# Kernel optimization log

Measured on AMD Instinct MI355X. Metric: run time of the kernel, lower is better.

Reference implementation:

```python
import jax, jax.numpy as jnp
import numpy as np

B, T, C, H = 4, 2048, 1024, 16
D = C // H  # head_dim = 64


def setup_inputs() -> dict:
    key = jax.random.key(0)
    k1, k2, k3 = jax.random.split(key, 3)
    x = jax.random.normal(k1, (B, T, C), dtype=jnp.float32)
    # torch Linear init ~ U(-1/sqrt(fan_in), 1/sqrt(fan_in)); scaled normal is fine for a baseline
    w_qkv = jax.random.normal(k2, (C, 3 * C), dtype=jnp.float32) * (1.0 / np.sqrt(C))
    w_proj = jax.random.normal(k3, (C, C), dtype=jnp.float32) * (1.0 / np.sqrt(C))
    return {"x": x, "w_qkv": w_qkv, "w_proj": w_proj}


def reference(x, w_qkv, w_proj):
    Bb, Tt, Cc = x.shape
    qkv = x @ w_qkv                                   # [B,T,3C]
    q, k, v = jnp.split(qkv, 3, axis=-1)
    # [B,T,C] -> [B,H,T,D]
    q = q.reshape(Bb, Tt, H, D).transpose(0, 2, 1, 3)
    k = k.reshape(Bb, Tt, H, D).transpose(0, 2, 1, 3)
    v = v.reshape(Bb, Tt, H, D).transpose(0, 2, 1, 3)
    scale = 1.0 / np.sqrt(D).astype(np.float32)
    logits = jnp.einsum("bhqd,bhkd->bhqk", q, k) * scale  # [B,H,T,T]
    causal = jnp.tril(jnp.ones((Tt, Tt), dtype=bool))
    logits = jnp.where(causal, logits, jnp.finfo(logits.dtype).min)
    attn = jax.nn.softmax(logits, axis=-1)
    y = jnp.einsum("bhqk,bhkd->bhqd", attn, v)            # [B,H,T,D]
    y = y.transpose(0, 2, 1, 3).reshape(Bb, Tt, Cc)
    return y @ w_proj                                     # dropout p=0 (eval)
```

## Files before the change

### kernel.cpp

```cpp
#include <hip/hip_runtime.h>
#include <hip/hip_bf16.h>
#include <stdint.h>

typedef unsigned short u16;
typedef __attribute__((ext_vector_type(4))) float f32x4;
typedef __attribute__((ext_vector_type(16))) float f32x16;
typedef __attribute__((ext_vector_type(8))) __bf16 bf16x8;
typedef __attribute__((ext_vector_type(2))) unsigned int u32x2;

__device__ __forceinline__ u16 f2bf(float f) {
  union { float f; uint32_t u; } x; x.f = f;
  const uint32_t u = x.u;
  return (u16)((u + 0x7fffu + ((u >> 16) & 1u)) >> 16);
}

#define QSCALE 0.1803368801111244f

__global__ void cvt_f32_bf16(const float* __restrict__ in, u16* __restrict__ out,
                             int n) {
  const int i = (blockIdx.x * blockDim.x + threadIdx.x) * 4;
  if (i < n) {
    const float4 v = *(const float4*)(in + i);
    ushort4 o;
    o.x = f2bf(v.x); o.y = f2bf(v.y); o.z = f2bf(v.z); o.w = f2bf(v.w);
    *(ushort4*)(out + i) = o;
  }
}

__global__ void transpose_cvt(const float* __restrict__ in, u16* __restrict__ out,
                              int R, int Cc) {
  __shared__ u16 tile[64][66];
  const int tx = threadIdx.x, ty = threadIdx.y;
  const int c0 = blockIdx.x * 64, r0 = blockIdx.y * 64;
#pragma unroll
  for (int i = 0; i < 4; ++i)
    tile[ty + i * 16][tx] = f2bf(in[(size_t)(r0 + ty + i * 16) * Cc + c0 + tx]);
  __syncthreads();
#pragma unroll
  for (int i = 0; i < 4; ++i)
    out[(size_t)(c0 + ty + i * 16) * R + r0 + tx] = tile[tx][ty + i * 16];
}

__global__ void transpose_v(const u16* __restrict__ V, u16* __restrict__ VT) {
  __shared__ u16 tile[64][66];
  const int tx = threadIdx.x, ty = threadIdx.y;
  const int r0 = blockIdx.x * 64;
  const size_t ho = (size_t)blockIdx.y * 2048 * 64;
  const u16* in = V + ho;
  u16* out = VT + ho;
#pragma unroll
  for (int i = 0; i < 4; ++i)
    tile[ty + i * 16][tx] = in[(size_t)(r0 + ty + i * 16) * 64 + tx];
  __syncthreads();
#pragma unroll
  for (int i = 0; i < 4; ++i)
    out[(size_t)(ty + i * 16) * 2048 + r0 + tx] = tile[tx][ty + i * 16];
}

__global__ __launch_bounds__(512, 2) void gemm8p_qkv(
    const u16* __restrict__ A, const u16* __restrict__ BT,
    u16* __restrict__ Qo, u16* __restrict__ Ko, u16* __restrict__ Vo,
    int K) {
  __shared__ u16 L[2][2][2][128 * 64];
  const int tid = threadIdx.x, wid = tid >> 6, lane = tid & 63;
  const int wm = wid >> 2, wn = wid & 3;
  const int l15 = lane & 15, l4 = lane >> 4;
  const int bn = blockIdx.x, bm = blockIdx.y;

  const u16* Atile = A + (size_t)bm * 256 * K;
  const u16* Btile = BT + (size_t)bn * 256 * K;

  f32x4 acc[8][4] = {};
  bf16x8 aF[4][2], bF[4][2];
  const int cb = wid * 64 + lane;

#define SB8() __builtin_amdgcn_sched_barrier(0)
#define BAR8() { SB8(); __builtin_amdgcn_s_barrier(); SB8(); }
#define VW4() { SB8(); asm volatile("s_waitcnt vmcnt(4)" ::: "memory"); SB8(); }
#define STG(d, op, h, kt) { \
    const u16* s0_ = ((op) ? Btile : Atile) + (size_t)(h) * 128 * K + (size_t)(kt) * 64; \
    _Pragma("unroll") for (int j_ = 0; j_ < 2; ++j_) { \
      const int c_ = j_ * 512 + cb; \
      const int r_ = c_ >> 3; \
      const int g_ = (c_ & 7) ^ (r_ & 7); \
      __builtin_amdgcn_global_load_lds( \
          (const __attribute__((address_space(1))) uint32_t*)(s0_ + (size_t)r_ * K + g_ * 8), \
          (__attribute__((address_space(3))) uint32_t*)(&L[d][op][h][(j_ * 512 + wid * 64) * 8]), 16, 0, 0); \
    } }
#define LD_A(d, mbase) { \
    _Pragma("unroll") for (int m_ = 0; m_ < 4; ++m_) \
    _Pragma("unroll") for (int k_ = 0; k_ < 2; ++k_) \
      aF[m_][k_] = *(const bf16x8*)&L[d][0][wm][(((mbase) + m_) * 16 + l15) * 64 + (((k_ * 4 + l4) ^ (l15 & 7)) * 8)]; }
#define LD_B(d, nbase) { \
    _Pragma("unroll") for (int n_ = 0; n_ < 2; ++n_) \
    _Pragma("unroll") for (int k_ = 0; k_ < 2; ++k_) \
      bF[(nbase) + n_][k_] = *(const bf16x8*)&L[d][1][wn >> 1][((wn & 1) * 64 + ((nbase) + n_) * 16 + l15) * 64 + (((k_ * 4 + l4) ^ (l15 & 7)) * 8)]; }
#define MQ(MS, NS) { __builtin_amdgcn_s_setprio(1); \
    _Pragma("unroll") for (int m_ = 0; m_ < 4; ++m_) \
    _Pragma("unroll") for (int n_ = 0; n_ < 2; ++n_) \
    _Pragma("unroll") for (int kk_ = 0; kk_ < 2; ++kk_) \
      acc[(MS) * 4 + m_][(NS) * 2 + n_] = __builtin_amdgcn_mfma_f32_16x16x32_bf16( \
          aF[m_][kk_], bF[(NS) * 2 + n_][kk_], acc[(MS) * 4 + m_][(NS) * 2 + n_], 0, 0, 0); \
    __builtin_amdgcn_s_setprio(0); }

  STG(0, 1, 0, 0); STG(0, 0, 0, 0); STG(0, 1, 1, 0); STG(0, 0, 1, 0);
  STG(1, 1, 0, 1); STG(1, 0, 0, 1);
  VW4();
  BAR8();

  const int nkt = K >> 6;
  for (int it = 0; it < nkt / 2; ++it) {
    const int t1 = 2 * it + 1;
    const int t2 = (2 * it + 2 < nkt) ? 2 * it + 2 : nkt - 1;
    const int t3 = (2 * it + 3 < nkt) ? 2 * it + 3 : nkt - 1;
    LD_A(0, 0); LD_B(0, 0);
    STG(1, 1, 1, t1);
    BAR8(); MQ(0, 0); BAR8();
    LD_B(0, 2);
    STG(1, 0, 1, t1);
    BAR8(); MQ(0, 1); BAR8();
    LD_A(0, 4);
    STG(0, 1, 0, t2);
    BAR8(); MQ(1, 0); BAR8();
    STG(0, 0, 0, t2);
    VW4();
    BAR8(); MQ(1, 1); BAR8();
    LD_A(1, 0); LD_B(1, 0);
    STG(0, 1, 1, t2);
    BAR8(); MQ(0, 0); BAR8();
    LD_B(1, 2);
    STG(0, 0, 1, t2);
    BAR8(); MQ(0, 1); BAR8();
    LD_A(1, 4);
    STG(1, 1, 0, t3);
    BAR8(); MQ(1, 0); BAR8();
    STG(1, 0, 0, t3);
    VW4();
    BAR8(); MQ(1, 1); BAR8();
  }
  asm volatile("s_waitcnt vmcnt(0)" ::: "memory");

  const int row0 = bm * 256 + wm * 128;
  const int col0 = bn * 256 + wn * 64;
#pragma unroll
  for (int m = 0; m < 8; ++m) {
#pragma unroll
    for (int n = 0; n < 4; ++n) {
#pragma unroll
      for (int jj = 0; jj < 4; ++jj) {
        const int row = row0 + m * 16 + l4 * 4 + jj;
        const int col = col0 + n * 16 + l15;
        const int sec = col >> 10, c = col & 1023;
        const int h = c >> 6, d = c & 63;
        const int b = row >> 11, t = row & 2047;
        float av = acc[m][n][jj];
        if (sec == 0) av *= QSCALE;
        u16* dst = (sec == 0) ? Qo : (sec == 1) ? Ko : Vo;
        dst[(((size_t)(b * 16 + h)) * 2048 + t) * 64 + d] = f2bf(av);
      }
    }
  }
#undef SB8
#undef BAR8
#undef VW4
#undef STG
#undef LD_A
#undef LD_B
#undef MQ
}

__global__ __launch_bounds__(256) void gemm_bt(
    const u16* __restrict__ A, const u16* __restrict__ BT,
    float* __restrict__ out, int M, int N, int K) {
  __shared__ u16 Asm_[128 * 32];
  __shared__ u16 Bsm_[128 * 32];
  const int tid = threadIdx.x;
  const int wid = tid >> 6, lane = tid & 63;
  const int wm = wid >> 1, wn = wid & 1;
  const int l15 = lane & 15, l4 = lane >> 4;
  const int bm = blockIdx.y, bn = blockIdx.x;

  const u16* Ag = A + (size_t)bm * 128 * K;
  const u16* Bg = BT + (size_t)bn * 128 * K;

  f32x4 acc[4][4] = {};

  const int srow = lane >> 2;
  const int scol = (lane & 3) * 8;

  for (int kt = 0; kt < K; kt += 32) {
    __syncthreads();
#pragma unroll
    for (int it = 0; it < 2; ++it) {
      const int c = it * 4 + wid;
      const int row = c * 16 + srow;
      __builtin_amdgcn_global_load_lds(
          (const __attribute__((address_space(1))) uint32_t*)(Ag + (size_t)row * K + kt + scol),
          (__attribute__((address_space(3))) uint32_t*)(&Asm_[c * 512]), 16, 0, 0);
      __builtin_amdgcn_global_load_lds(
          (const __attribute__((address_space(1))) uint32_t*)(Bg + (size_t)row * K + kt + scol),
          (__attribute__((address_space(3))) uint32_t*)(&Bsm_[c * 512]), 16, 0, 0);
    }
    __syncthreads();

    bf16x8 af[4], bfr[4];
#pragma unroll
    for (int m = 0; m < 4; ++m)
      af[m] = *(const bf16x8*)&Asm_[(wm * 64 + m * 16 + l15) * 32 + l4 * 8];
#pragma unroll
    for (int n = 0; n < 4; ++n)
      bfr[n] = *(const bf16x8*)&Bsm_[(wn * 64 + n * 16 + l15) * 32 + l4 * 8];
#pragma unroll
    for (int m = 0; m < 4; ++m)
#pragma unroll
      for (int n = 0; n < 4; ++n)
        acc[m][n] = __builtin_amdgcn_mfma_f32_16x16x32_bf16(af[m], bfr[n], acc[m][n], 0, 0, 0);
  }

  const int row0 = bm * 128 + wm * 64;
  const int col0 = bn * 128 + wn * 64;
#pragma unroll
  for (int m = 0; m < 4; ++m)
#pragma unroll
    for (int n = 0; n < 4; ++n)
#pragma unroll
      for (int j = 0; j < 4; ++j) {
        const int row = row0 + m * 16 + l4 * 4 + j;
        const int col = col0 + n * 16 + l15;
        out[(size_t)row * N + col] = acc[m][n][j];
      }
}

__global__ __launch_bounds__(256, 4) void attn_fwd(const u16* __restrict__ Qp,
                                                   const u16* __restrict__ Kp,
                                                   const u16* __restrict__ VTp,
                                                   u16* __restrict__ Y) {
  constexpr int DP = 72;
  constexpr float THR = 11.0f;
  __shared__ u16 Ks[2][64 * DP];
  __shared__ u16 Vt[2][64 * DP];

  const int xorm = (int)((0x0A050F00u >> ((blockIdx.y >> 4) * 8)) & 15u);
  const int qt = (int)blockIdx.x ^ xorm;
  const int bh = blockIdx.y;
  const int b = bh >> 4, h = bh & 15;
  const int tid = threadIdx.x, lane = tid & 63;
  const int wid = tid >> 6;
  const int l31 = lane & 31, hb = lane >> 5;

  const size_t head_off = (size_t)bh * 2048 * 64;
  const u16* Kh = Kp + head_off;
  const u16* VTh = VTp + head_off;

  const int qg = qt * 128 + wid * 32 + l31;
  const u16* Qrow = Qp + head_off + (size_t)qg * 64;

  bf16x8 qf[4];
#pragma unroll
  for (int d = 0; d < 4; ++d)
    qf[d] = *(const bf16x8*)(Qrow + d * 16 + hb * 8);

  float m_ = -1e30f, l_ = 0.f;
  f32x16 oacc[2] = {};

  const int sr = tid >> 3;
  const int sc = (tid & 7) * 8;

  bf16x8 kreg[2], vreg[2];
  auto kvload = [&](int kt) {
#pragma unroll
    for (int it = 0; it < 2; ++it) {
      const int r = sr + it * 32;
      kreg[it] = *(const bf16x8*)(Kh + (size_t)(kt * 64 + r) * 64 + sc);
      vreg[it] = *(const bf16x8*)(VTh + (size_t)r * 2048 + kt * 64 + sc);
    }
  };
  auto kvwrite = [&](int buf) {
#pragma unroll
    for (int it = 0; it < 2; ++it) {
      const int r = sr + it * 32;
      *(bf16x8*)&Ks[buf][r * DP + sc] = kreg[it];
      *(bf16x8*)&Vt[buf][r * DP + sc] = vreg[it];
    }
  };

  kvload(0);
  kvwrite(0);
  __syncthreads();

  const int nt = 2 * qt + 2;
  for (int kt = 0; kt < nt; ++kt) {
    const int cur = kt & 1;
    const bool havenext = (kt + 1 < nt);
    if (havenext) kvload(kt + 1);

    const bool diag = (kt >= 2 * qt);

#pragma unroll
    for (int kb2 = 0; kb2 < 2; ++kb2) {
      f32x16 s = {};
      __builtin_amdgcn_s_setprio(1);
#pragma unroll
      for (int d = 0; d < 4; ++d) {
        const bf16x8 kf = *(const bf16x8*)&Ks[cur][(kb2 * 32 + l31) * DP + d * 16 + hb * 8];
        s = __builtin_amdgcn_mfma_f32_32x32x16_bf16(kf, qf[d], s, 0, 0, 0);
      }
      __builtin_amdgcn_s_setprio(0);

      if (diag) {
        const int kbase = kt * 64 + kb2 * 32 + hb * 4;
#pragma unroll
        for (int r = 0; r < 16; ++r) {
          const int koff = (r & 3) + 8 * (r >> 2);
          if (kbase + koff > qg) s[r] = -1e30f;
        }
      }

      float pmax = s[0];
#pragma unroll
      for (int r = 1; r < 16; ++r) pmax = fmaxf(pmax, s[r]);
      if (!__all(pmax - m_ <= THR)) {
        const float fm = fmaxf(pmax, __shfl_xor(pmax, 32));
        const float mnew = fmaxf(m_, fm);
        const float alpha = __builtin_exp2f(m_ - mnew);
        m_ = mnew;
        l_ *= alpha;
#pragma unroll
        for (int nb = 0; nb < 2; ++nb)
#pragma unroll
          for (int r = 0; r < 16; ++r) oacc[nb][r] *= alpha;
      }
#pragma unroll
      for (int r = 0; r < 16; ++r) {
        s[r] = __builtin_exp2f(s[r] - m_);
        l_ += s[r];
      }

      bf16x8 pb[2];
#pragma unroll
      for (int st = 0; st < 2; ++st) {
        uint32_t x0, x1, y0, y1;
        asm("v_cvt_pk_bf16_f32 %0, %1, %2" : "=v"(x0) : "v"(s[8 * st + 0]), "v"(s[8 * st + 1]));
        asm("v_cvt_pk_bf16_f32 %0, %1, %2" : "=v"(x1) : "v"(s[8 * st + 2]), "v"(s[8 * st + 3]));
        asm("v_cvt_pk_bf16_f32 %0, %1, %2" : "=v"(y0) : "v"(s[8 * st + 4]), "v"(s[8 * st + 5]));
        asm("v_cvt_pk_bf16_f32 %0, %1, %2" : "=v"(y1) : "v"(s[8 * st + 6]), "v"(s[8 * st + 7]));
        const u32x2 r0 = __builtin_amdgcn_permlane32_swap(x0, y0, false, false);
        const u32x2 r1 = __builtin_amdgcn_permlane32_swap(x1, y1, false, false);
        union { uint32_t w[4]; bf16x8 v; } u;
        u.w[0] = r0[0]; u.w[1] = r1[0]; u.w[2] = r0[1]; u.w[3] = r1[1];
        pb[st] = u.v;
      }

      __builtin_amdgcn_s_setprio(1);
#pragma unroll
      for (int nb = 0; nb < 2; ++nb)
#pragma unroll
        for (int st = 0; st < 2; ++st) {
          const bf16x8 vf = *(const bf16x8*)&Vt[cur][(nb * 32 + l31) * DP + kb2 * 32 + st * 16 + hb * 8];
          oacc[nb] = __builtin_amdgcn_mfma_f32_32x32x16_bf16(vf, pb[st], oacc[nb], 0, 0, 0);
        }
      __builtin_amdgcn_s_setprio(0);
    }

    if (havenext) kvwrite(cur ^ 1);
    __syncthreads();
  }

  const float lf = l_ + __shfl_xor(l_, 32);
  const float inv = 1.0f / lf;
  u16* Yrow = Y + ((size_t)b * 2048 + qg) * 1024 + h * 64;
#pragma unroll
  for (int nb = 0; nb < 2; ++nb) {
#pragma unroll
    for (int g = 0; g < 4; ++g) {
      ushort4 o;
      o.x = f2bf(oacc[nb][4 * g + 0] * inv);
      o.y = f2bf(oacc[nb][4 * g + 1] * inv);
      o.z = f2bf(oacc[nb][4 * g + 2] * inv);
      o.w = f2bf(oacc[nb][4 * g + 3] * inv);
      *(ushort4*)(Yrow + nb * 32 + g * 8 + hb * 4) = o;
    }
  }
}

extern "C" void kernel_launch(void* const* d_in, const int* in_sizes, int n_in,
                              void* d_out, int out_size, void* d_ws,
                              size_t ws_size, hipStream_t stream) {
  const float* x = (const float*)d_in[0];
  const float* w_qkv = (const float*)d_in[1];
  const float* w_proj = (const float*)d_in[2];
  float* out = (float*)d_out;

  char* ws = (char*)d_ws;
  u16* xb = (u16*)ws;
  u16* VTw = (u16*)ws;
  u16* wqkvT = (u16*)(ws + 16777216);
  u16* wprojT = (u16*)(ws + 23068672);
  u16* Qw = (u16*)(ws + 25165824);
  u16* Kw = (u16*)(ws + 41943040);
  u16* Vw = (u16*)(ws + 58720256);
  u16* Yw = (u16*)(ws + 75497472);
  if (ws_size < 92274688) return;

  cvt_f32_bf16<<<dim3(8192), dim3(256), 0, stream>>>(x, xb, 8388608);

  dim3 tb(64, 16);
  transpose_cvt<<<dim3(48, 16), tb, 0, stream>>>(w_qkv, wqkvT, 1024, 3072);
  transpose_cvt<<<dim3(16, 16), tb, 0, stream>>>(w_proj, wprojT, 1024, 1024);

  gemm8p_qkv<<<dim3(12, 32), dim3(512), 0, stream>>>(
      xb, wqkvT, Qw, Kw, Vw, 1024);

  transpose_v<<<dim3(32, 64), tb, 0, stream>>>(Vw, VTw);

  attn_fwd<<<dim3(16, 64), dim3(256), 0, stream>>>(Qw, Kw, VTw, Yw);

  gemm_bt<<<dim3(8, 64), dim3(256), 0, stream>>>(
      Yw, wprojT, out, 8192, 1024, 1024);
}
```

Baseline: 193.8 us.

## Shrink QKV GEMM tile to 128x256 and double the grid

Changes the QKV projection GEMM block tile from 256x256 to 128x256, halving the A-tile LDS buffer and accumulator registers, and rewrites the staging and MFMA schedule to match. The grid doubles to 768 blocks, which fills the 256 CUs more evenly than 384 blocks did and lowers LDS and register use per block. The cost is less data reuse per block, so B tiles are read from global memory twice as often.

```diff
diff --git a/kernel.cpp b/kernel.cpp
--- a/kernel.cpp
+++ b/kernel.cpp
@@ -61,50 +61,53 @@
     const u16* __restrict__ A, const u16* __restrict__ BT,
     u16* __restrict__ Qo, u16* __restrict__ Ko, u16* __restrict__ Vo,
     int K) {
-  __shared__ u16 L[2][2][2][128 * 64];
+  __shared__ u16 LA[2][128 * 64];
+  __shared__ u16 LB[2][2][128 * 64];
   const int tid = threadIdx.x, wid = tid >> 6, lane = tid & 63;
   const int wm = wid >> 2, wn = wid & 3;
   const int l15 = lane & 15, l4 = lane >> 4;
   const int bn = blockIdx.x, bm = blockIdx.y;
 
-  const u16* Atile = A + (size_t)bm * 256 * K;
+  const u16* Atile = A + (size_t)bm * 128 * K;
   const u16* Btile = BT + (size_t)bn * 256 * K;
 
-  f32x4 acc[8][4] = {};
+  f32x4 acc[4][4] = {};
   bf16x8 aF[4][2], bF[4][2];
   const int cb = wid * 64 + lane;
 
 #define SB8() __builtin_amdgcn_sched_barrier(0)
 #define BAR8() { SB8(); __builtin_amdgcn_s_barrier(); SB8(); }
 #define VW4() { SB8(); asm volatile("s_waitcnt vmcnt(4)" ::: "memory"); SB8(); }
-#define STG(d, op, h, kt) { \
-    const u16* s0_ = ((op) ? Btile : Atile) + (size_t)(h) * 128 * K + (size_t)(kt) * 64; \
+#define STGU(dst, srcbase) { \
+    const u16* s0_ = (srcbase); \
     _Pragma("unroll") for (int j_ = 0; j_ < 2; ++j_) { \
       const int c_ = j_ * 512 + cb; \
       const int r_ = c_ >> 3; \
       const int g_ = (c_ & 7) ^ (r_ & 7); \
       __builtin_amdgcn_global_load_lds( \
           (const __attribute__((address_space(1))) uint32_t*)(s0_ + (size_t)r_ * K + g_ * 8), \
-          (__attribute__((address_space(3))) uint32_t*)(&L[d][op][h][(j_ * 512 + wid * 64) * 8]), 16, 0, 0); \
+          (__attribute__((address_space(3))) uint32_t*)(&(dst)[(j_ * 512 + wid * 64) * 8]), 16, 0, 0); \
     } }
-#define LD_A(d, mbase) { \
+#define STG_A(d, kt) STGU(LA[d], Atile + (size_t)(kt) * 64)
+#define STG_B(d, h, kt) STGU(LB[d][h], Btile + (size_t)(h) * 128 * K + (size_t)(kt) * 64)
+#define LD_A(d) { \
     _Pragma("unroll") for (int m_ = 0; m_ < 4; ++m_) \
     _Pragma("unroll") for (int k_ = 0; k_ < 2; ++k_) \
-      aF[m_][k_] = *(const bf16x8*)&L[d][0][wm][(((mbase) + m_) * 16 + l15) * 64 + (((k_ * 4 + l4) ^ (l15 & 7)) * 8)]; }
+      aF[m_][k_] = *(const bf16x8*)&LA[d][(wm * 64 + m_ * 16 + l15) * 64 + (((k_ * 4 + l4) ^ (l15 & 7)) * 8)]; }
 #define LD_B(d, nbase) { \
     _Pragma("unroll") for (int n_ = 0; n_ < 2; ++n_) \
     _Pragma("unroll") for (int k_ = 0; k_ < 2; ++k_) \
-      bF[(nbase) + n_][k_] = *(const bf16x8*)&L[d][1][wn >> 1][((wn & 1) * 64 + ((nbase) + n_) * 16 + l15) * 64 + (((k_ * 4 + l4) ^ (l15 & 7)) * 8)]; }
+      bF[(nbase) + n_][k_] = *(const bf16x8*)&LB[d][wn >> 1][((wn & 1) * 64 + ((nbase) + n_) * 16 + l15) * 64 + (((k_ * 4 + l4) ^ (l15 & 7)) * 8)]; }
 #define MQ(MS, NS) { __builtin_amdgcn_s_setprio(1); \
-    _Pragma("unroll") for (int m_ = 0; m_ < 4; ++m_) \
+    _Pragma("unroll") for (int m_ = 0; m_ < 2; ++m_) \
     _Pragma("unroll") for (int n_ = 0; n_ < 2; ++n_) \
     _Pragma("unroll") for (int kk_ = 0; kk_ < 2; ++kk_) \
-      acc[(MS) * 4 + m_][(NS) * 2 + n_] = __builtin_amdgcn_mfma_f32_16x16x32_bf16( \
-          aF[m_][kk_], bF[(NS) * 2 + n_][kk_], acc[(MS) * 4 + m_][(NS) * 2 + n_], 0, 0, 0); \
+      acc[(MS) * 2 + m_][(NS) * 2 + n_] = __builtin_amdgcn_mfma_f32_16x16x32_bf16( \
+          aF[(MS) * 2 + m_][kk_], bF[(NS) * 2 + n_][kk_], acc[(MS) * 2 + m_][(NS) * 2 + n_], 0, 0, 0); \
     __builtin_amdgcn_s_setprio(0); }
 
-  STG(0, 1, 0, 0); STG(0, 0, 0, 0); STG(0, 1, 1, 0); STG(0, 0, 1, 0);
-  STG(1, 1, 0, 1); STG(1, 0, 0, 1);
+  STG_A(0, 0); STG_B(0, 0, 0); STG_B(0, 1, 0);
+  STG_A(1, 1); STG_B(1, 0, 1);
   VW4();
   BAR8();
 
@@ -113,37 +116,33 @@
     const int t1 = 2 * it + 1;
     const int t2 = (2 * it + 2 < nkt) ? 2 * it + 2 : nkt - 1;
     const int t3 = (2 * it + 3 < nkt) ? 2 * it + 3 : nkt - 1;
-    LD_A(0, 0); LD_B(0, 0);
-    STG(1, 1, 1, t1);
+    LD_A(0); LD_B(0, 0);
+    STG_B(1, 1, t1);
     BAR8(); MQ(0, 0); BAR8();
+    STG_A(0, t2);
+    BAR8(); MQ(1, 0); BAR8();
     LD_B(0, 2);
-    STG(1, 0, 1, t1);
     BAR8(); MQ(0, 1); BAR8();
-    LD_A(0, 4);
-    STG(0, 1, 0, t2);
-    BAR8(); MQ(1, 0); BAR8();
-    STG(0, 0, 0, t2);
+    STG_B(0, 0, t2);
     VW4();
     BAR8(); MQ(1, 1); BAR8();
-    LD_A(1, 0); LD_B(1, 0);
-    STG(0, 1, 1, t2);
+    LD_A(1); LD_B(1, 0);
+    STG_B(0, 1, t2);
     BAR8(); MQ(0, 0); BAR8();
+    STG_A(1, t3);
+    BAR8(); MQ(1, 0); BAR8();
     LD_B(1, 2);
-    STG(0, 0, 1, t2);
     BAR8(); MQ(0, 1); BAR8();
-    LD_A(1, 4);
-    STG(1, 1, 0, t3);
-    BAR8(); MQ(1, 0); BAR8();
-    STG(1, 0, 0, t3);
+    STG_B(1, 0, t3);
     VW4();
     BAR8(); MQ(1, 1); BAR8();
   }
   asm volatile("s_waitcnt vmcnt(0)" ::: "memory");
 
-  const int row0 = bm * 256 + wm * 128;
+  const int row0 = bm * 128 + wm * 64;
   const int col0 = bn * 256 + wn * 64;
 #pragma unroll
-  for (int m = 0; m < 8; ++m) {
+  for (int m = 0; m < 4; ++m) {
 #pragma unroll
     for (int n = 0; n < 4; ++n) {
 #pragma unroll
@@ -163,7 +162,9 @@
 #undef SB8
 #undef BAR8
 #undef VW4
-#undef STG
+#undef STGU
+#undef STG_A
+#undef STG_B
 #undef LD_A
 #undef LD_B
 #undef MQ
@@ -408,7 +409,7 @@
   transpose_cvt<<<dim3(48, 16), tb, 0, stream>>>(w_qkv, wqkvT, 1024, 3072);
   transpose_cvt<<<dim3(16, 16), tb, 0, stream>>>(w_proj, wprojT, 1024, 1024);
 
-  gemm8p_qkv<<<dim3(12, 32), dim3(512), 0, stream>>>(
+  gemm8p_qkv<<<dim3(12, 64), dim3(512), 0, stream>>>(
       xb, wqkvT, Qw, Kw, Vw, 1024);
 
   transpose_v<<<dim3(32, 64), tb, 0, stream>>>(Vw, VTw);
```

Result: no change. 197.5 us, median of 2 (+1.9%).
